# Kernel tuning notes

Measured on AMD Instinct MI355X. Metric: run time of the kernel, lower is better.

## Reference

```python
import jax, jax.numpy as jnp
import numpy as np

HIDDEN = 4096
FFN = 11008
N_HEADS = 32
HEAD_DIM = HIDDEN // N_HEADS
BATCH = 1
SEQLEN = 1024
PAST = 1024
ROPE_BASE = 10000.0
EPS = 1e-6


def rms_norm(x, w, eps=EPS):
    var = jnp.mean(x * x, axis=-1, keepdims=True)
    return x * jax.lax.rsqrt(var + eps) * w


def rope(x):
    # x: (b, h, s, d); concatenated-halves variant: [e*cos - o*sin, e*sin + o*cos]
    s, d = x.shape[-2], x.shape[-1]
    pos = jnp.arange(s, dtype=x.dtype)[:, None]                      # (s, 1)
    freqs = ROPE_BASE ** (-jnp.arange(0, d, 2, dtype=x.dtype) / d)   # (d/2,)
    ang = pos * freqs                                                # (s, d/2)
    cos, sin = jnp.cos(ang), jnp.sin(ang)
    xe, xo = x[..., ::2], x[..., 1::2]
    return jnp.concatenate([xe * cos - xo * sin, xe * sin + xo * cos], axis=-1)


def setup_inputs() -> dict:
    key = jax.random.key(0)
    ks = jax.random.split(key, 9)
    sc = 0.02
    return {
        "x": jax.random.normal(ks[0], (BATCH, SEQLEN, HIDDEN), jnp.float32),
        "wq": jax.random.normal(ks[1], (HIDDEN, HIDDEN), jnp.float32) * sc,
        "wk": jax.random.normal(ks[2], (HIDDEN, HIDDEN), jnp.float32) * sc,
        "wv": jax.random.normal(ks[3], (HIDDEN, HIDDEN), jnp.float32) * sc,
        "wo": jax.random.normal(ks[4], (HIDDEN, HIDDEN), jnp.float32) * sc,
        "w1": jax.random.normal(ks[5], (FFN, HIDDEN), jnp.float32) * sc,
        "w2": jax.random.normal(ks[6], (HIDDEN, FFN), jnp.float32) * sc,
        "w3": jax.random.normal(ks[7], (FFN, HIDDEN), jnp.float32) * sc,
        "attn_norm_w": jnp.ones((HIDDEN,), jnp.float32),
        "ffn_norm_w": jnp.ones((HIDDEN,), jnp.float32),
        "past_k": jnp.zeros((BATCH, N_HEADS, PAST, HEAD_DIM), jnp.float32),
        "past_v": jnp.zeros((BATCH, N_HEADS, PAST, HEAD_DIM), jnp.float32),
    }


def reference(x, wq, wk, wv, wo, w1, w2, w3, attn_norm_w, ffn_norm_w, past_k, past_v):
    bsz, seqlen, _ = x.shape
    h = rms_norm(x, attn_norm_w)
    # projections: nn.Linear -> h @ W^T, reshape to (b, n_heads, s, d)
    def split_heads(y):
        return y.reshape(bsz, seqlen, N_HEADS, HEAD_DIM).transpose(0, 2, 1, 3)
    xq = split_heads(h @ wq.T)
    xk = split_heads(h @ wk.T)
    xv = split_heads(h @ wv.T)
    xq = rope(xq)
    xk = rope(xk)  # computed but unused downstream (faithful to source)
    # attention against the KV-cache buffers (zeros); no scaling, no mask
    scores_raw = jnp.einsum('bhsd,bhpd->bhsp', xq, past_k)
    scores = jax.nn.softmax(scores_raw, axis=-1)
    out = jnp.einsum('bhsp,bhpd->bhsd', scores, past_v)
    out = out.transpose(0, 2, 1, 3).reshape(bsz, seqlen, -1)
    xo = out @ wo.T
    # SwiGLU FFN (no residuals in source)
    hf = rms_norm(xo, ffn_norm_w)
    x1 = hf @ w1.T
    x3 = jax.nn.silu(hf @ w3.T)
    return (x1 * x3) @ w2.T
```

## Files before the change

### kernel.cpp

```cpp
#include <hip/hip_runtime.h>
#include <hip/hip_bf16.h>


typedef __attribute__((ext_vector_type(4))) float  floatx4;
typedef __attribute__((ext_vector_type(8))) __bf16 bf16x8;
typedef __attribute__((ext_vector_type(4))) __bf16 bf16x4;

#define HIDDEN 4096
#define FFN    11008
#define SEQLEN 1024
#define NHEADS 32
#define HDIM   128
#define PAST   1024

__device__ __forceinline__ void gload_lds16(const void* g, void* l) {
    __builtin_amdgcn_global_load_lds(
        (const __attribute__((address_space(1))) void*)g,
        (__attribute__((address_space(3))) void*)l, 16, 0, 0);
}

__global__ __launch_bounds__(256) void rmsnorm_bf16(
    const float* __restrict__ x, const float* __restrict__ w,
    __bf16* __restrict__ out)
{
    const int row = blockIdx.x;
    const float* xr = x + (size_t)row * HIDDEN;
    float4 v[4];
    float ss = 0.f;
#pragma unroll
    for (int i = 0; i < 4; ++i) {
        v[i] = *(const float4*)(xr + threadIdx.x * 4 + i * 1024);
        ss += v[i].x * v[i].x + v[i].y * v[i].y + v[i].z * v[i].z + v[i].w * v[i].w;
    }
#pragma unroll
    for (int off = 32; off > 0; off >>= 1) ss += __shfl_down(ss, off);
    __shared__ float red[4];
    if ((threadIdx.x & 63) == 0) red[threadIdx.x >> 6] = ss;
    __syncthreads();
    float total = red[0] + red[1] + red[2] + red[3];
    float scale = rsqrtf(total * (1.f / HIDDEN) + 1e-6f);
#pragma unroll
    for (int i = 0; i < 4; ++i) {
        int idx = threadIdx.x * 4 + i * 1024;
        float4 wv = *(const float4*)(w + idx);
        bf16x4 o;
        o[0] = (__bf16)(v[i].x * scale * wv.x);
        o[1] = (__bf16)(v[i].y * scale * wv.y);
        o[2] = (__bf16)(v[i].z * scale * wv.z);
        o[3] = (__bf16)(v[i].w * scale * wv.w);
        *(bf16x4*)(out + (size_t)row * HIDDEN + idx) = o;
    }
}

template<int SPLIT>
__global__ __launch_bounds__(256, 2) void gemm2(
    const __bf16* __restrict__ A, const float* __restrict__ W,
    float* __restrict__ C, int M, int N, int K)
{
    __shared__ __bf16 Asb[2][128 * 64];
    __shared__ __bf16 Bsb[2][128 * 72];

    const int tid  = threadIdx.x;
    const int wave = tid >> 6;
    const int lane = tid & 63;
    const int l15  = lane & 15;
    const int quad = lane >> 4;
    const int wr   = wave >> 1;
    const int wc   = wave & 1;

    const int nwg = gridDim.x;
    int flat = blockIdx.x;
    int q = nwg >> 3, r = nwg & 7;
    int xcd = flat & 7, ii = flat >> 3;
    int nf = (xcd < r) ? (xcd * (q + 1) + ii) : (r * (q + 1) + (xcd - r) * q + ii);
    const int gm = M >> 7;
    const int bn = nf / gm, bm = nf - bn * gm;

    const int Kper  = K / SPLIT;
    const int kbase = blockIdx.y * Kper;
    const int nt    = Kper >> 6;

    const int arow = (lane >> 3);
    const int akb  = ((lane & 7) * 16) ^ ((lane >> 3) << 4);
    const __bf16* Abase = A + (size_t)(bm * 128) * K + kbase + (akb >> 1);

    const int wrow = tid >> 1, wh = tid & 1;
    const float* Wbase = W + (size_t)(bn * 128 + wrow) * K + kbase + wh * 32;

    floatx4 acc[4][4] = {};
    float4 wreg[8];

    {
#pragma unroll
        for (int j = 0; j < 8; ++j)
            wreg[j] = *(const float4*)(Wbase + j * 4);
#pragma unroll
        for (int i = 0; i < 4; ++i) {
            int c = wave * 4 + i;
            gload_lds16(Abase + (size_t)(c * 8 + arow) * K, &Asb[0][c * 512]);
        }
#pragma unroll
        for (int j = 0; j < 4; ++j) {
            bf16x8 b;
            b[0] = (__bf16)wreg[2*j].x;   b[1] = (__bf16)wreg[2*j].y;
            b[2] = (__bf16)wreg[2*j].z;   b[3] = (__bf16)wreg[2*j].w;
            b[4] = (__bf16)wreg[2*j+1].x; b[5] = (__bf16)wreg[2*j+1].y;
            b[6] = (__bf16)wreg[2*j+1].z; b[7] = (__bf16)wreg[2*j+1].w;
            *(bf16x8*)(&Bsb[0][wrow * 72 + wh * 32 + j * 8]) = b;
        }
        __syncthreads();
    }

    for (int t = 0; t < nt; ++t) {
        const int cur = t & 1, nxt = cur ^ 1;
        const bool more = (t + 1 < nt);

        if (more) {
            const float* wb = Wbase + (t + 1) * 64;
#pragma unroll
            for (int j = 0; j < 8; ++j)
                wreg[j] = *(const float4*)(wb + j * 4);
            const __bf16* ab = Abase + (t + 1) * 64;
#pragma unroll
            for (int i = 0; i < 4; ++i) {
                int c = wave * 4 + i;
                gload_lds16(ab + (size_t)(c * 8 + arow) * K, &Asb[nxt][c * 512]);
            }
        }

#pragma unroll
        for (int kk = 0; kk < 2; ++kk) {
            bf16x8 af[4], bfr[4];
#pragma unroll
            for (int i = 0; i < 4; ++i) {
                int R  = wr * 64 + i * 16 + l15;
                int kb = (kk * 64 + quad * 16) ^ ((l15 & 7) << 4);
                af[i] = *(const bf16x8*)((const char*)&Asb[cur][R * 64] + kb);
            }
#pragma unroll
            for (int j = 0; j < 4; ++j) {
                int R2 = wc * 64 + j * 16 + l15;
                bfr[j] = *(const bf16x8*)(&Bsb[cur][R2 * 72 + kk * 32 + quad * 8]);
            }
#pragma unroll
            for (int i = 0; i < 4; ++i)
#pragma unroll
                for (int j = 0; j < 4; ++j)
                    acc[i][j] = __builtin_amdgcn_mfma_f32_16x16x32_bf16(af[i], bfr[j], acc[i][j], 0, 0, 0);
        }

        if (more) {
#pragma unroll
            for (int j = 0; j < 4; ++j) {
                bf16x8 b;
                b[0] = (__bf16)wreg[2*j].x;   b[1] = (__bf16)wreg[2*j].y;
                b[2] = (__bf16)wreg[2*j].z;   b[3] = (__bf16)wreg[2*j].w;
                b[4] = (__bf16)wreg[2*j+1].x; b[5] = (__bf16)wreg[2*j+1].y;
                b[6] = (__bf16)wreg[2*j+1].z; b[7] = (__bf16)wreg[2*j+1].w;
                *(bf16x8*)(&Bsb[nxt][wrow * 72 + wh * 32 + j * 8]) = b;
            }
            __syncthreads();
        }
    }

    float* Co = (SPLIT > 1) ? (C + (size_t)blockIdx.y * M * N) : C;
#pragma unroll
    for (int i = 0; i < 4; ++i) {
        int mrow = bm * 128 + wr * 64 + i * 16 + quad * 4;
#pragma unroll
        for (int j = 0; j < 4; ++j) {
            int ncol = bn * 128 + wc * 64 + j * 16 + l15;
            float* cp = Co + (size_t)mrow * N + ncol;
#pragma unroll
            for (int rr = 0; rr < 4; ++rr)
                cp[(size_t)rr * N] = acc[i][j][rr];
        }
    }
}

__global__ __launch_bounds__(256) void rope_table(float* __restrict__ tab)
{
    int idx = blockIdx.x * 256 + threadIdx.x;
    int s = idx >> 6, j = idx & 63;
    float freq = __powf(10000.f, -(float)(2 * j) * (1.f / 128.f));
    float sn, cs;
    __sincosf((float)s * freq, &sn, &cs);
    tab[2 * idx]     = cs;
    tab[2 * idx + 1] = sn;
}

__global__ __launch_bounds__(256) void combine_rope(
    const float* __restrict__ p, const float* __restrict__ tab,
    __bf16* __restrict__ out)
{
    const int s = blockIdx.x;
    const float* r0 = p + (size_t)s * HIDDEN;
    const float* r1 = r0 + (size_t)SEQLEN * HIDDEN;
    __bf16* orow = out + (size_t)s * HIDDEN;
    for (int pi = threadIdx.x; pi < 2048; pi += 256) {
        int h = pi >> 6, j = pi & 63;
        int base = h * 128;
        float2 e0 = *(const float2*)(r0 + base + 2 * j);
        float2 e1 = *(const float2*)(r1 + base + 2 * j);
        float xe = e0.x + e1.x, xo = e0.y + e1.y;
        float2 cs = *(const float2*)(tab + (size_t)s * 128 + 2 * j);
        orow[base + j]      = (__bf16)(xe * cs.x - xo * cs.y);
        orow[base + 64 + j] = (__bf16)(xe * cs.y + xo * cs.x);
    }
}

__global__ __launch_bounds__(256) void combine_add(
    const float* __restrict__ p, float* __restrict__ out, int n)
{
    int i = (blockIdx.x * 256 + threadIdx.x) * 4;
    float4 a = *(const float4*)(p + i);
    float4 b = *(const float4*)(p + n + i);
    float4 o; o.x = a.x + b.x; o.y = a.y + b.y; o.z = a.z + b.z; o.w = a.w + b.w;
    *(float4*)(out + i) = o;
}

__global__ __launch_bounds__(256) void attn_flash(
    const __bf16* __restrict__ q, const float* __restrict__ pk,
    const float* __restrict__ pv, __bf16* __restrict__ out)
{
    const int qt = blockIdx.x;
    const int h  = blockIdx.y;
    const int s0 = qt * 64;
    const int tid  = threadIdx.x;
    const int wave = tid >> 6;
    const int lane = tid & 63;
    const int l15  = lane & 15;
    const int quad = lane >> 4;

    __shared__ __bf16 Ks[64 * 136];
    __shared__ __bf16 Vt[128 * 72];
    __shared__ __bf16 Ps[64 * 72];

    bf16x8 qf[4];
    {
        const __bf16* qrow = q + (size_t)(s0 + wave * 16 + l15) * HIDDEN + h * HDIM;
#pragma unroll
        for (int ks = 0; ks < 4; ++ks)
            qf[ks] = *(const bf16x8*)(qrow + ks * 32 + quad * 8);
    }

    floatx4 Oa[8] = {};
    float m_r[4], l_r[4];
#pragma unroll
    for (int r = 0; r < 4; ++r) { m_r[r] = -1e30f; l_r[r] = 0.f; }

    for (int p0 = 0; p0 < PAST; p0 += 64) {
        const float* kbase = pk + ((size_t)h * PAST + p0) * HDIM;
        const float* vbase = pv + ((size_t)h * PAST + p0) * HDIM;
#pragma unroll
        for (int i = 0; i < 8; ++i) {
            int f = i * 256 + tid;
            int p = f >> 5, dq = (f & 31) * 4;
            float4 k4 = *(const float4*)(kbase + p * HDIM + dq);
            bf16x4 kb;
            kb[0] = (__bf16)k4.x; kb[1] = (__bf16)k4.y;
            kb[2] = (__bf16)k4.z; kb[3] = (__bf16)k4.w;
            *(bf16x4*)(&Ks[p * 136 + dq]) = kb;
            float4 v4 = *(const float4*)(vbase + p * HDIM + dq);
            Vt[(dq + 0) * 72 + p] = (__bf16)v4.x;
            Vt[(dq + 1) * 72 + p] = (__bf16)v4.y;
            Vt[(dq + 2) * 72 + p] = (__bf16)v4.z;
            Vt[(dq + 3) * 72 + p] = (__bf16)v4.w;
        }
        __syncthreads();

        floatx4 Sa[4] = {};
#pragma unroll
        for (int nb = 0; nb < 4; ++nb)
#pragma unroll
            for (int ks = 0; ks < 4; ++ks) {
                bf16x8 kf = *(const bf16x8*)(&Ks[(nb * 16 + l15) * 136 + ks * 32 + quad * 8]);
                Sa[nb] = __builtin_amdgcn_mfma_f32_16x16x32_bf16(qf[ks], kf, Sa[nb], 0, 0, 0);
            }

        float mnew[4];
#pragma unroll
        for (int r = 0; r < 4; ++r) {
            float t = fmaxf(fmaxf(Sa[0][r], Sa[1][r]), fmaxf(Sa[2][r], Sa[3][r]));
#pragma unroll
            for (int off = 1; off < 16; off <<= 1) t = fmaxf(t, __shfl_xor(t, off));
            mnew[r] = fmaxf(m_r[r], t);
        }
#pragma unroll
        for (int r = 0; r < 4; ++r) {
            float alpha = __expf(m_r[r] - mnew[r]);
            m_r[r] = mnew[r];
            float s = 0.f;
#pragma unroll
            for (int nb = 0; nb < 4; ++nb) {
                float e = __expf(Sa[nb][r] - mnew[r]);
                Sa[nb][r] = e;
                s += e;
            }
#pragma unroll
            for (int off = 1; off < 16; off <<= 1) s += __shfl_xor(s, off);
            l_r[r] = l_r[r] * alpha + s;
#pragma unroll
            for (int nb = 0; nb < 8; ++nb) Oa[nb][r] *= alpha;
        }

#pragma unroll
        for (int nb = 0; nb < 4; ++nb)
#pragma unroll
            for (int r = 0; r < 4; ++r)
                Ps[(wave * 16 + quad * 4 + r) * 72 + nb * 16 + l15] = (__bf16)Sa[nb][r];

#pragma unroll
        for (int ks2 = 0; ks2 < 2; ++ks2) {
            bf16x8 pf = *(const bf16x8*)(&Ps[(wave * 16 + l15) * 72 + ks2 * 32 + quad * 8]);
#pragma unroll
            for (int nb = 0; nb < 8; ++nb) {
                bf16x8 vf = *(const bf16x8*)(&Vt[(nb * 16 + l15) * 72 + ks2 * 32 + quad * 8]);
                Oa[nb] = __builtin_amdgcn_mfma_f32_16x16x32_bf16(pf, vf, Oa[nb], 0, 0, 0);
            }
        }
        __syncthreads();
    }

    float inv[4];
#pragma unroll
    for (int r = 0; r < 4; ++r) inv[r] = 1.f / l_r[r];
#pragma unroll
    for (int nb = 0; nb < 8; ++nb)
#pragma unroll
        for (int r = 0; r < 4; ++r)
            out[(size_t)(s0 + wave * 16 + quad * 4 + r) * HIDDEN + h * HDIM + nb * 16 + l15] =
                (__bf16)(Oa[nb][r] * inv[r]);
}

__global__ __launch_bounds__(256) void silu_mul_bf16(
    const float* __restrict__ x1, const float* __restrict__ x3,
    __bf16* __restrict__ out)
{
    int i = (blockIdx.x * 256 + threadIdx.x) * 4;
    float4 a = *(const float4*)(x1 + i);
    float4 b = *(const float4*)(x3 + i);
    bf16x4 o;
    o[0] = (__bf16)(a.x * (b.x / (1.f + __expf(-b.x))));
    o[1] = (__bf16)(a.y * (b.y / (1.f + __expf(-b.y))));
    o[2] = (__bf16)(a.z * (b.z / (1.f + __expf(-b.z))));
    o[3] = (__bf16)(a.w * (b.w / (1.f + __expf(-b.w))));
    *(bf16x4*)(out + i) = o;
}

extern "C" void kernel_launch(void* const* d_in, const int* in_sizes, int n_in,
                              void* d_out, int out_size, void* d_ws, size_t ws_size,
                              hipStream_t stream)
{
    const float* x   = (const float*)d_in[0];
    const float* wq  = (const float*)d_in[1];
    const float* wo  = (const float*)d_in[4];
    const float* w1  = (const float*)d_in[5];
    const float* w2  = (const float*)d_in[6];
    const float* w3  = (const float*)d_in[7];
    const float* anw = (const float*)d_in[8];
    const float* fnw = (const float*)d_in[9];
    const float* pk  = (const float*)d_in[10];
    const float* pv  = (const float*)d_in[11];
    float* out = (float*)d_out;

    char* ws = (char*)d_ws;
    constexpr size_t MB  = 1ull << 20;
    constexpr size_t HMB = 512ull << 10;
    float*  tab   = (float*)(ws);
    __bf16* h_bf  = (__bf16*)(ws + HMB);
    float*  qp    = (float*)(ws + HMB + 8  * MB);
    __bf16* xq_bf = (__bf16*)(ws + HMB);
    __bf16* ao_bf = (__bf16*)(ws + HMB + 8  * MB);
    float*  op    = (float*)(ws + HMB + 16 * MB);
    float*  xo    = (float*)(ws + HMB);
    __bf16* hf_bf = (__bf16*)(ws + HMB + 48 * MB);
    float*  x1    = (float*)(ws + HMB);
    float*  x3    = (float*)(ws + HMB + 56 * MB);
    __bf16* g_bf  = (__bf16*)(ws + HMB + 102 * MB);
    float*  w2p   = (float*)(ws + HMB);

    rope_table<<<256, 256, 0, stream>>>(tab);
    rmsnorm_bf16<<<SEQLEN, 256, 0, stream>>>(x, anw, h_bf);
    gemm2<2><<<dim3((HIDDEN / 128) * (SEQLEN / 128), 2), 256, 0, stream>>>(
        h_bf, wq, qp, SEQLEN, HIDDEN, HIDDEN);
    combine_rope<<<SEQLEN, 256, 0, stream>>>(qp, tab, xq_bf);
    attn_flash<<<dim3(SEQLEN / 64, NHEADS), 256, 0, stream>>>(xq_bf, pk, pv, ao_bf);
    gemm2<2><<<dim3((HIDDEN / 128) * (SEQLEN / 128), 2), 256, 0, stream>>>(
        ao_bf, wo, op, SEQLEN, HIDDEN, HIDDEN);
    combine_add<<<(SEQLEN * HIDDEN) / 1024, 256, 0, stream>>>(op, xo, SEQLEN * HIDDEN);
    rmsnorm_bf16<<<SEQLEN, 256, 0, stream>>>(xo, fnw, hf_bf);
    gemm2<1><<<dim3((FFN / 128) * (SEQLEN / 128), 1), 256, 0, stream>>>(
        hf_bf, w1, x1, SEQLEN, FFN, HIDDEN);
    gemm2<1><<<dim3((FFN / 128) * (SEQLEN / 128), 1), 256, 0, stream>>>(
        hf_bf, w3, x3, SEQLEN, FFN, HIDDEN);
    silu_mul_bf16<<<(SEQLEN * FFN) / 1024, 256, 0, stream>>>(x1, x3, g_bf);
    gemm2<2><<<dim3((HIDDEN / 128) * (SEQLEN / 128), 2), 256, 0, stream>>>(
        g_bf, w2, w2p, SEQLEN, HIDDEN, FFN);
    combine_add<<<(SEQLEN * HIDDEN) / 1024, 256, 0, stream>>>(w2p, out, SEQLEN * HIDDEN);
}
```

Measured before the change: 1.619 ms.

## Stream fp32 weights straight to LDS and raise split-K to four

The GEMM is restructured. The fp32 weight tile now goes directly into LDS through global_load_lds with an XOR swizzle, instead of being staged in registers and converted to bf16 before the LDS store. The bf16 conversion moves to the LDS read path. The K tile shrinks to 32 and double buffering is dropped, in exchange for fewer registers and a target of 4 workgroups per CU to hide latency through occupancy. The square projections now use split-K of 4 with matching 4-way combine kernels, and workspace offsets are relaid to fit the larger partial buffers. The risks are more barrier stalls without prefetch overlap, doubled fp32 LDS traffic, and extra partial-sum memory traffic.

```diff
diff --git a/kernel.cpp b/kernel.cpp
--- a/kernel.cpp
+++ b/kernel.cpp
@@ -53,12 +53,12 @@
 }
 
 template<int SPLIT>
-__global__ __launch_bounds__(256, 2) void gemm2(
+__global__ __launch_bounds__(256, 4) void gemm3(
     const __bf16* __restrict__ A, const float* __restrict__ W,
     float* __restrict__ C, int M, int N, int K)
 {
-    __shared__ __bf16 Asb[2][128 * 64];
-    __shared__ __bf16 Bsb[2][128 * 72];
+    __shared__ __align__(16) __bf16 As[128 * 32];
+    __shared__ __align__(16) float  Bs[128 * 32];
 
     const int tid  = threadIdx.x;
     const int wave = tid >> 6;
@@ -71,96 +71,64 @@
     const int nwg = gridDim.x;
     int flat = blockIdx.x;
     int q = nwg >> 3, r = nwg & 7;
-    int xcd = flat & 7, ii = flat >> 3;
-    int nf = (xcd < r) ? (xcd * (q + 1) + ii) : (r * (q + 1) + (xcd - r) * q + ii);
+    int xcd = flat & 7, ii0 = flat >> 3;
+    int nf = (xcd < r) ? (xcd * (q + 1) + ii0) : (r * (q + 1) + (xcd - r) * q + ii0);
     const int gm = M >> 7;
     const int bn = nf / gm, bm = nf - bn * gm;
 
     const int Kper  = K / SPLIT;
-    const int kbase = blockIdx.y * Kper;
-    const int nt    = Kper >> 6;
-
-    const int arow = (lane >> 3);
-    const int akb  = ((lane & 7) * 16) ^ ((lane >> 3) << 4);
-    const __bf16* Abase = A + (size_t)(bm * 128) * K + kbase + (akb >> 1);
-
-    const int wrow = tid >> 1, wh = tid & 1;
-    const float* Wbase = W + (size_t)(bn * 128 + wrow) * K + kbase + wh * 32;
+    const int kbase = (SPLIT > 1) ? blockIdx.y * Kper : 0;
+    const int nt    = Kper >> 5;
+
+    const int a_kb = ((lane & 3) * 16) ^ (((lane >> 2) & 3) << 4);
+    const __bf16* Ag0 = A + (size_t)(bm * 128 + wave * 32 + (lane >> 2)) * K
+                          + kbase + (a_kb >> 1);
+    const __bf16* Ag1 = Ag0 + (size_t)16 * K;
+    char* Al = (char*)As + wave * 2048;
+
+    const int b_kb = ((lane & 7) * 16) ^ ((lane >> 3) << 4);
+    const float* Wg = W + (size_t)(bn * 128 + wave * 32 + (lane >> 3)) * K
+                        + kbase + (b_kb >> 2);
+    char* Bl = (char*)Bs + wave * 4096;
 
     floatx4 acc[4][4] = {};
-    float4 wreg[8];
-
-    {
-#pragma unroll
-        for (int j = 0; j < 8; ++j)
-            wreg[j] = *(const float4*)(Wbase + j * 4);
+
+    for (int t = 0; t < nt; ++t) {
+        const int ko = t * 32;
+        gload_lds16(Ag0 + ko, Al);
+        gload_lds16(Ag1 + ko, Al + 1024);
+#pragma unroll
+        for (int i = 0; i < 4; ++i)
+            gload_lds16(Wg + (size_t)(8 * i) * K + ko, Bl + i * 1024);
+        __syncthreads();
+
+        bf16x8 af[4], bfr[4];
 #pragma unroll
         for (int i = 0; i < 4; ++i) {
-            int c = wave * 4 + i;
-            gload_lds16(Abase + (size_t)(c * 8 + arow) * K, &Asb[0][c * 512]);
+            int R = wr * 64 + i * 16 + l15;
+            af[i] = *(const bf16x8*)((const char*)As + R * 64
+                                     + ((quad * 16) ^ ((R & 3) << 4)));
         }
 #pragma unroll
         for (int j = 0; j < 4; ++j) {
+            int R2 = wc * 64 + j * 16 + l15;
+            const char* bp = (const char*)Bs + R2 * 128;
+            float4 lo = *(const float4*)(bp + ((quad * 32) ^ ((R2 & 7) << 4)));
+            float4 hi = *(const float4*)(bp + ((quad * 32 + 16) ^ ((R2 & 7) << 4)));
             bf16x8 b;
-            b[0] = (__bf16)wreg[2*j].x;   b[1] = (__bf16)wreg[2*j].y;
-            b[2] = (__bf16)wreg[2*j].z;   b[3] = (__bf16)wreg[2*j].w;
-            b[4] = (__bf16)wreg[2*j+1].x; b[5] = (__bf16)wreg[2*j+1].y;
-            b[6] = (__bf16)wreg[2*j+1].z; b[7] = (__bf16)wreg[2*j+1].w;
-            *(bf16x8*)(&Bsb[0][wrow * 72 + wh * 32 + j * 8]) = b;
-        }
+            b[0] = (__bf16)lo.x; b[1] = (__bf16)lo.y;
+            b[2] = (__bf16)lo.z; b[3] = (__bf16)lo.w;
+            b[4] = (__bf16)hi.x; b[5] = (__bf16)hi.y;
+            b[6] = (__bf16)hi.z; b[7] = (__bf16)hi.w;
+            bfr[j] = b;
+        }
+#pragma unroll
+        for (int i = 0; i < 4; ++i)
+#pragma unroll
+            for (int j = 0; j < 4; ++j)
+                acc[i][j] = __builtin_amdgcn_mfma_f32_16x16x32_bf16(
+                    af[i], bfr[j], acc[i][j], 0, 0, 0);
         __syncthreads();
-    }
-
-    for (int t = 0; t < nt; ++t) {
-        const int cur = t & 1, nxt = cur ^ 1;
-        const bool more = (t + 1 < nt);
-
-        if (more) {
-            const float* wb = Wbase + (t + 1) * 64;
-#pragma unroll
-            for (int j = 0; j < 8; ++j)
-                wreg[j] = *(const float4*)(wb + j * 4);
-            const __bf16* ab = Abase + (t + 1) * 64;
-#pragma unroll
-            for (int i = 0; i < 4; ++i) {
-                int c = wave * 4 + i;
-                gload_lds16(ab + (size_t)(c * 8 + arow) * K, &Asb[nxt][c * 512]);
-            }
-        }
-
-#pragma unroll
-        for (int kk = 0; kk < 2; ++kk) {
-            bf16x8 af[4], bfr[4];
-#pragma unroll
-            for (int i = 0; i < 4; ++i) {
-                int R  = wr * 64 + i * 16 + l15;
-                int kb = (kk * 64 + quad * 16) ^ ((l15 & 7) << 4);
-                af[i] = *(const bf16x8*)((const char*)&Asb[cur][R * 64] + kb);
-            }
-#pragma unroll
-            for (int j = 0; j < 4; ++j) {
-                int R2 = wc * 64 + j * 16 + l15;
-                bfr[j] = *(const bf16x8*)(&Bsb[cur][R2 * 72 + kk * 32 + quad * 8]);
-            }
-#pragma unroll
-            for (int i = 0; i < 4; ++i)
-#pragma unroll
-                for (int j = 0; j < 4; ++j)
-                    acc[i][j] = __builtin_amdgcn_mfma_f32_16x16x32_bf16(af[i], bfr[j], acc[i][j], 0, 0, 0);
-        }
-
-        if (more) {
-#pragma unroll
-            for (int j = 0; j < 4; ++j) {
-                bf16x8 b;
-                b[0] = (__bf16)wreg[2*j].x;   b[1] = (__bf16)wreg[2*j].y;
-                b[2] = (__bf16)wreg[2*j].z;   b[3] = (__bf16)wreg[2*j].w;
-                b[4] = (__bf16)wreg[2*j+1].x; b[5] = (__bf16)wreg[2*j+1].y;
-                b[6] = (__bf16)wreg[2*j+1].z; b[7] = (__bf16)wreg[2*j+1].w;
-                *(bf16x8*)(&Bsb[nxt][wrow * 72 + wh * 32 + j * 8]) = b;
-            }
-            __syncthreads();
-        }
     }
 
     float* Co = (SPLIT > 1) ? (C + (size_t)blockIdx.y * M * N) : C;
@@ -189,33 +157,42 @@
     tab[2 * idx + 1] = sn;
 }
 
-__global__ __launch_bounds__(256) void combine_rope(
+__global__ __launch_bounds__(256) void combine_rope4(
     const float* __restrict__ p, const float* __restrict__ tab,
     __bf16* __restrict__ out)
 {
     const int s = blockIdx.x;
+    const size_t n = (size_t)SEQLEN * HIDDEN;
     const float* r0 = p + (size_t)s * HIDDEN;
-    const float* r1 = r0 + (size_t)SEQLEN * HIDDEN;
     __bf16* orow = out + (size_t)s * HIDDEN;
     for (int pi = threadIdx.x; pi < 2048; pi += 256) {
         int h = pi >> 6, j = pi & 63;
         int base = h * 128;
         float2 e0 = *(const float2*)(r0 + base + 2 * j);
-        float2 e1 = *(const float2*)(r1 + base + 2 * j);
-        float xe = e0.x + e1.x, xo = e0.y + e1.y;
+        float2 e1 = *(const float2*)(r0 + n + base + 2 * j);
+        float2 e2 = *(const float2*)(r0 + 2 * n + base + 2 * j);
+        float2 e3 = *(const float2*)(r0 + 3 * n + base + 2 * j);
+        float xe = e0.x + e1.x + e2.x + e3.x;
+        float xo = e0.y + e1.y + e2.y + e3.y;
         float2 cs = *(const float2*)(tab + (size_t)s * 128 + 2 * j);
         orow[base + j]      = (__bf16)(xe * cs.x - xo * cs.y);
         orow[base + 64 + j] = (__bf16)(xe * cs.y + xo * cs.x);
     }
 }
 
-__global__ __launch_bounds__(256) void combine_add(
+__global__ __launch_bounds__(256) void combine_add4(
     const float* __restrict__ p, float* __restrict__ out, int n)
 {
     int i = (blockIdx.x * 256 + threadIdx.x) * 4;
     float4 a = *(const float4*)(p + i);
-    float4 b = *(const float4*)(p + n + i);
-    float4 o; o.x = a.x + b.x; o.y = a.y + b.y; o.z = a.z + b.z; o.w = a.w + b.w;
+    float4 b = *(const float4*)(p + (size_t)n + i);
+    float4 c = *(const float4*)(p + 2 * (size_t)n + i);
+    float4 d = *(const float4*)(p + 3 * (size_t)n + i);
+    float4 o;
+    o.x = a.x + b.x + c.x + d.x;
+    o.y = a.y + b.y + c.y + d.y;
+    o.z = a.z + b.z + c.z + d.z;
+    o.w = a.w + b.w + c.w + d.w;
     *(float4*)(out + i) = o;
 }
 
@@ -365,37 +342,36 @@
     float* out = (float*)d_out;
 
     char* ws = (char*)d_ws;
-    constexpr size_t MB  = 1ull << 20;
-    constexpr size_t HMB = 512ull << 10;
+    constexpr size_t MB = 1ull << 20;
     float*  tab   = (float*)(ws);
-    __bf16* h_bf  = (__bf16*)(ws + HMB);
-    float*  qp    = (float*)(ws + HMB + 8  * MB);
-    __bf16* xq_bf = (__bf16*)(ws + HMB);
-    __bf16* ao_bf = (__bf16*)(ws + HMB + 8  * MB);
-    float*  op    = (float*)(ws + HMB + 16 * MB);
-    float*  xo    = (float*)(ws + HMB);
-    __bf16* hf_bf = (__bf16*)(ws + HMB + 48 * MB);
-    float*  x1    = (float*)(ws + HMB);
-    float*  x3    = (float*)(ws + HMB + 56 * MB);
-    __bf16* g_bf  = (__bf16*)(ws + HMB + 102 * MB);
-    float*  w2p   = (float*)(ws + HMB);
+    __bf16* h_bf  = (__bf16*)(ws + 1 * MB);
+    float*  qp    = (float*)(ws + 9 * MB);
+    __bf16* xq_bf = (__bf16*)(ws + 1 * MB);
+    __bf16* ao_bf = (__bf16*)(ws + 9 * MB);
+    float*  op    = (float*)(ws + 17 * MB);
+    float*  xo    = (float*)(ws + 1 * MB);
+    __bf16* hf_bf = (__bf16*)(ws + 96 * MB);
+    float*  x1    = (float*)(ws + 1 * MB);
+    float*  x3    = (float*)(ws + 47 * MB);
+    __bf16* g_bf  = (__bf16*)(ws + 104 * MB);
+    float*  w2p   = (float*)(ws + 1 * MB);
 
     rope_table<<<256, 256, 0, stream>>>(tab);
     rmsnorm_bf16<<<SEQLEN, 256, 0, stream>>>(x, anw, h_bf);
-    gemm2<2><<<dim3((HIDDEN / 128) * (SEQLEN / 128), 2), 256, 0, stream>>>(
+    gemm3<4><<<dim3((HIDDEN / 128) * (SEQLEN / 128), 4), 256, 0, stream>>>(
         h_bf, wq, qp, SEQLEN, HIDDEN, HIDDEN);
-    combine_rope<<<SEQLEN, 256, 0, stream>>>(qp, tab, xq_bf);
+    combine_rope4<<<SEQLEN, 256, 0, stream>>>(qp, tab, xq_bf);
     attn_flash<<<dim3(SEQLEN / 64, NHEADS), 256, 0, stream>>>(xq_bf, pk, pv, ao_bf);
-    gemm2<2><<<dim3((HIDDEN / 128) * (SEQLEN / 128), 2), 256, 0, stream>>>(
+    gemm3<4><<<dim3((HIDDEN / 128) * (SEQLEN / 128), 4), 256, 0, stream>>>(
         ao_bf, wo, op, SEQLEN, HIDDEN, HIDDEN);
-    combine_add<<<(SEQLEN * HIDDEN) / 1024, 256, 0, stream>>>(op, xo, SEQLEN * HIDDEN);
+    combine_add4<<<(SEQLEN * HIDDEN) / 1024, 256, 0, stream>>>(op, xo, SEQLEN * HIDDEN);
     rmsnorm_bf16<<<SEQLEN, 256, 0, stream>>>(xo, fnw, hf_bf);
-    gemm2<1><<<dim3((FFN / 128) * (SEQLEN / 128), 1), 256, 0, stream>>>(
+    gemm3<1><<<dim3((FFN / 128) * (SEQLEN / 128), 1), 256, 0, stream>>>(
         hf_bf, w1, x1, SEQLEN, FFN, HIDDEN);
-    gemm2<1><<<dim3((FFN / 128) * (SEQLEN / 128), 1), 256, 0, stream>>>(
+    gemm3<1><<<dim3((FFN / 128) * (SEQLEN / 128), 1), 256, 0, stream>>>(
         hf_bf, w3, x3, SEQLEN, FFN, HIDDEN);
     silu_mul_bf16<<<(SEQLEN * FFN) / 1024, 256, 0, stream>>>(x1, x3, g_bf);
-    gemm2<2><<<dim3((HIDDEN / 128) * (SEQLEN / 128), 2), 256, 0, stream>>>(
+    gemm3<4><<<dim3((HIDDEN / 128) * (SEQLEN / 128), 4), 256, 0, stream>>>(
         g_bf, w2, w2p, SEQLEN, HIDDEN, FFN);
-    combine_add<<<(SEQLEN * HIDDEN) / 1024, 256, 0, stream>>>(w2p, out, SEQLEN * HIDDEN);
-}
+    combine_add4<<<(SEQLEN * HIDDEN) / 1024, 256, 0, stream>>>(w2p, out, SEQLEN * HIDDEN);
+}
```

Result: faster. 1.378 ms (-14.9%).
